# Optimization experiments

Measured on AMD Instinct MI355X. Metric: run time of the kernel, lower is better.

The kernel has to match this reference:

```python
import jax, jax.numpy as jnp
import numpy as np

EPS = 1e-8      # F.normalize eps in _cos_angle
TOPK = 4
DELTA = 1.0     # huber delta
EXTRA_FRAMES = (1, 3, 5, 7)            # teacher-only frames
SHARED = ((2, 1), (4, 2), (6, 3))      # (teacher_idx, student_idx) for shared frames


def _huber(e):
    ae = jnp.abs(e)
    return jnp.where(ae <= DELTA, 0.5 * e * e, DELTA * (ae - 0.5 * DELTA))


def _angles(R, H, Sh):
    # R: [b,r,d] ref, H: [b,r,k,d] sim_high, Sh: [b,s,d] shared.
    # Cosines of the three triplet angles computed via dot-product expansion,
    # avoiding any [b,r,s,k,d] intermediate. cos = (u.v)/(max(|u|,eps)*max(|v|,eps))
    RH  = jnp.einsum('brd,brkd->brk', R, H)
    RSh = jnp.einsum('brd,bsd->brs', R, Sh)
    HSh = jnp.einsum('brkd,bsd->brsk', H, Sh)
    Rn2  = jnp.sum(R * R, -1)        # [b,r]
    Hn2  = jnp.sum(H * H, -1)        # [b,r,k]
    Shn2 = jnp.sum(Sh * Sh, -1)      # [b,s]
    n_RSh = jnp.maximum(jnp.sqrt(jnp.maximum(Rn2[:, :, None] + Shn2[:, None, :] - 2 * RSh, 0.0)), EPS)          # |R-Sh| [b,r,s]
    n_RH  = jnp.maximum(jnp.sqrt(jnp.maximum(Rn2[:, :, None] + Hn2 - 2 * RH, 0.0)), EPS)                        # |R-H|  [b,r,k]
    n_HSh = jnp.maximum(jnp.sqrt(jnp.maximum(Hn2[:, :, None, :] + Shn2[:, None, :, None] - 2 * HSh, 0.0)), EPS) # |H-Sh| [b,r,s,k]
    # angle1: vertex=ref, u=Sh-R, v=H-R
    d1 = HSh - RSh[..., None] - RH[:, :, None, :] + Rn2[:, :, None, None]
    a1 = d1 / (n_RSh[..., None] * n_RH[:, :, None, :])
    # angle2: vertex=H, u=R-H, v=Sh-H
    d2 = RSh[..., None] - RH[:, :, None, :] - HSh + Hn2[:, :, None, :]
    a2 = d2 / (n_RH[:, :, None, :] * n_HSh)
    # angle3: vertex=Sh, u=R-Sh, v=H-Sh
    d3 = RH[:, :, None, :] - RSh[..., None] - HSh + Shn2[:, None, :, None]
    a3 = d3 / (n_RSh[..., None] * n_HSh)
    return a1, a2, a3


def setup_inputs() -> dict:
    key = jax.random.key(0)
    k1, k2, k3, k4 = jax.random.split(key, 4)
    B, S_T, P, D = 2, 8, 2048, 1024
    num_ref, num_shared = 128, 128
    teacher_feats = jax.random.normal(k1, (B, S_T, P, D), jnp.float32)
    student_feats = jax.random.normal(k2, (B, 4, P, D), jnp.float32)
    ref_perm = jax.random.permutation(k3, P)[:num_ref].astype(jnp.int32)
    shared_perm = jax.random.permutation(k4, P)[:num_shared].astype(jnp.int32)
    return {"teacher_feats": teacher_feats, "student_feats": student_feats,
            "ref_perm": ref_perm, "shared_perm": shared_perm}


def reference(teacher_feats, student_feats, ref_perm, shared_perm):
    tf = jax.lax.stop_gradient(teacher_feats)  # teacher is fully detached
    B, _, P, D = tf.shape
    num_ref = ref_perm.shape[0]
    num_shared = shared_perm.shape[0]
    ref_t = tf[:, 0, ref_perm, :]                 # [B,R,D]
    ref_s = student_feats[:, 0, ref_perm, :]
    # teacher-only frames, concatenated along patch dim -> [B, EP, D]
    extra = tf[:, jnp.array(EXTRA_FRAMES), :, :].reshape(B, -1, D)
    # cosine-similarity retrieval (selection_mode='topk')
    rtn = ref_t / jnp.maximum(jnp.linalg.norm(ref_t, axis=-1, keepdims=True), 1e-12)
    etn = extra / jnp.maximum(jnp.linalg.norm(extra, axis=-1, keepdims=True), 1e-12)
    sim = jnp.einsum('brd,bed->bre', rtn, etn)
    _, idx = jax.lax.top_k(sim, TOPK)             # [B,R,K]
    H = jnp.take_along_axis(extra, idx.reshape(B, -1, 1), axis=1).reshape(B, num_ref, TOPK, D)
    s1 = s2 = s3 = jnp.float32(0.0)
    for tidx, sidx in SHARED:
        Sh_t = tf[:, tidx, shared_perm, :]
        Sh_s = student_feats[:, sidx, shared_perm, :]
        a1t, a2t, a3t = _angles(ref_t, H, Sh_t)
        a1s, a2s, a3s = _angles(ref_s, H, Sh_s)
        s1 = s1 + _huber(a1s - a1t).sum()
        s2 = s2 + _huber(a2s - a2t).sum()
        s3 = s3 + _huber(a3s - a3t).sum()
    total = jnp.float32(len(SHARED) * B * num_ref * num_shared * TOPK)
    # angle weights all 1.0
    loss = s1 / total + s2 / total + s3 / total
    return loss
```

## Files before the change

### kernel.cpp

```cpp
#include <hip/hip_runtime.h>
#include <cstdint>
#include <cstddef>
#include <cfloat>
#include <climits>

#define D_DIM   1024
#define P_DIM   2048
#define NB      2
#define NR      128
#define NS      128
#define KTOP    4
#define E_DIM   8192
#define ANG_EPS 1e-8f
#define M_PAIR  768
#define N_PAIR  768

#define SIM_SLICES  4
#define SIM_KSLICE  256
#define PAIR_SLICES 4
#define PAIR_KSLICE 256
#define PAIR_STAGES 16

#define TOPK_DELTA  1.0f
#define MAXCAND     128

typedef short short8 __attribute__((ext_vector_type(8)));
typedef float f32x4 __attribute__((ext_vector_type(4)));

__device__ __forceinline__ float dot4(float4 a, float4 b) {
  return a.x * b.x + a.y * b.y + a.z * b.z + a.w * b.w;
}

__device__ __forceinline__ float huber(float e) {
  float ae = fabsf(e);
  return ae <= 1.0f ? 0.5f * e * e : ae - 0.5f;
}

__device__ __forceinline__ bool better(float va, int ia, float vb, int ib) {
  return (va > vb) || (va == vb && ia < ib);
}

__device__ __forceinline__ unsigned int f2bf(float x) {
  union { float f; unsigned int u; } v; v.f = x;
  unsigned int r = v.u + 0x7fffu + ((v.u >> 16) & 1u);
  return r >> 16;
}
__device__ __forceinline__ unsigned int pk2bf(float x, float y) {
  return f2bf(x) | (f2bf(y) << 16);
}

__device__ __forceinline__ float block_reduce_sum(float v, float* scratch) {
  #pragma unroll
  for (int o = 32; o > 0; o >>= 1) v += __shfl_down(v, o);
  __syncthreads();
  if ((threadIdx.x & 63) == 0) scratch[threadIdx.x >> 6] = v;
  __syncthreads();
  float r = 0.0f;
  int nw = (int)(blockDim.x >> 6);
  if ((int)threadIdx.x < nw) r = scratch[threadIdx.x];
  #pragma unroll
  for (int o = 2; o > 0; o >>= 1) r += __shfl_down(r, o);
  return r;
}

__global__ __launch_bounds__(256) void sim_gemm_kernel(const float* __restrict__ tf,
                                                       const int* __restrict__ ref_perm,
                                                       float* __restrict__ simP,
                                                       float* __restrict__ bn2P) {
  __shared__ unsigned int Ah[128 * 20];
  __shared__ unsigned int Bh[128 * 20];
  __shared__ const float* Arow[128];
  __shared__ const float* Brow[128];
  const int tid = threadIdx.x;
  const int b = blockIdx.z;
  const int slice = blockIdx.y;
  const int nbase = blockIdx.x * 128;
  const int kbase = slice * SIM_KSLICE;
  if (tid < 128) {
    Arow[tid] = tf + ((size_t)(b * 8) * P_DIM + ref_perm[tid]) * D_DIM + kbase;
  } else {
    int n = nbase + (tid - 128);
    Brow[tid - 128] = tf + ((size_t)(b * 8 + 1 + 2 * (n >> 11)) * P_DIM + (n & (P_DIM - 1))) * D_DIM + kbase;
  }
  __syncthreads();

  const int srow = tid >> 1;
  const int shalf = (tid & 1) * 16;
  const float* asrc = Arow[srow] + shalf;
  const float* bsrc = Brow[srow] + shalf;

  float4 av[4], bv[4];
  #pragma unroll
  for (int i = 0; i < 4; ++i) {
    av[i] = *(const float4*)(asrc + 4 * i);
    bv[i] = *(const float4*)(bsrc + 4 * i);
  }

  const int wave = tid >> 6;
  const int lane = tid & 63;
  const int fr = lane & 15;
  const int q16 = (lane >> 4) * 16;
  const char* Ab = (const char*)Ah;
  const char* Bb = (const char*)Bh;

  f32x4 acc[2][8];
  #pragma unroll
  for (int mt = 0; mt < 2; ++mt)
    #pragma unroll
    for (int nt = 0; nt < 8; ++nt)
      #pragma unroll
      for (int r = 0; r < 4; ++r) acc[mt][nt][r] = 0.0f;

  float bn2 = 0.0f;
  unsigned int* adst = Ah + srow * 20 + (tid & 1) * 8;
  unsigned int* bdst = Bh + srow * 20 + (tid & 1) * 8;

  for (int ck = 0; ck < 8; ++ck) {
    bn2 += dot4(bv[0], bv[0]) + dot4(bv[1], bv[1]) + dot4(bv[2], bv[2]) + dot4(bv[3], bv[3]);
    unsigned int ua[8], ub[8];
    #pragma unroll
    for (int i = 0; i < 4; ++i) {
      ua[2 * i]     = pk2bf(av[i].x, av[i].y);
      ua[2 * i + 1] = pk2bf(av[i].z, av[i].w);
      ub[2 * i]     = pk2bf(bv[i].x, bv[i].y);
      ub[2 * i + 1] = pk2bf(bv[i].z, bv[i].w);
    }
    __syncthreads();
    *(uint4*)(adst)     = make_uint4(ua[0], ua[1], ua[2], ua[3]);
    *(uint4*)(adst + 4) = make_uint4(ua[4], ua[5], ua[6], ua[7]);
    *(uint4*)(bdst)     = make_uint4(ub[0], ub[1], ub[2], ub[3]);
    *(uint4*)(bdst + 4) = make_uint4(ub[4], ub[5], ub[6], ub[7]);
    __syncthreads();
    if (ck < 7) {
      const float* an = asrc + (ck + 1) * 32;
      const float* bn = bsrc + (ck + 1) * 32;
      #pragma unroll
      for (int i = 0; i < 4; ++i) {
        av[i] = *(const float4*)(an + 4 * i);
        bv[i] = *(const float4*)(bn + 4 * i);
      }
    }
    short8 afr[2], bfr[8];
    #pragma unroll
    for (int mt = 0; mt < 2; ++mt)
      afr[mt] = *(const short8*)(Ab + (wave * 32 + mt * 16 + fr) * 80 + q16);
    #pragma unroll
    for (int nt = 0; nt < 8; ++nt)
      bfr[nt] = *(const short8*)(Bb + (nt * 16 + fr) * 80 + q16);
    #pragma unroll
    for (int mt = 0; mt < 2; ++mt)
      #pragma unroll
      for (int nt = 0; nt < 8; ++nt)
        acc[mt][nt] = __builtin_amdgcn_mfma_f32_16x16x32_bf16(afr[mt], bfr[nt], acc[mt][nt], 0, 0, 0);
  }

  bn2 += __shfl_xor(bn2, 1);
  if ((tid & 1) == 0)
    bn2P[((size_t)slice * NB + b) * E_DIM + nbase + srow] = bn2;

  float* base = simP + (((size_t)slice * NB + b) * NR) * E_DIM + nbase;
  const int crow = (lane >> 4) * 4;
  #pragma unroll
  for (int mt = 0; mt < 2; ++mt) {
    #pragma unroll
    for (int nt = 0; nt < 8; ++nt) {
      int col = nt * 16 + fr;
      #pragma unroll
      for (int r = 0; r < 4; ++r) {
        int m = wave * 32 + mt * 16 + crow + r;
        base[(size_t)m * E_DIM + col] = acc[mt][nt][r];
      }
    }
  }
}

__global__ __launch_bounds__(256) void topk_kernel(const float* __restrict__ simP,
                                                   const float* __restrict__ bn2P,
                                                   const float* __restrict__ tf,
                                                   const int* __restrict__ ref_perm,
                                                   int* __restrict__ tki) {
  __shared__ float scores[E_DIM];
  __shared__ float sv[1024];
  __shared__ int si[1024];
  __shared__ float candVal[MAXCAND];
  __shared__ int candIdx[MAXCAND];
  __shared__ int cnt;
  const int tid = threadIdx.x;
  const int br = blockIdx.x;
  const int b = br >> 7;
  const int r = br & 127;
  const size_t ST = (size_t)NB * NR * E_DIM;
  const size_t SN = (size_t)NB * E_DIM;
  const float* p = simP + (size_t)br * E_DIM;
  const float* q = bn2P + (size_t)b * E_DIM;
  if (tid == 0) cnt = 0;

  float tv[4] = {-FLT_MAX, -FLT_MAX, -FLT_MAX, -FLT_MAX};
  int ti[4] = {INT_MAX, INT_MAX, INT_MAX, INT_MAX};
  for (int e4 = tid * 4; e4 < E_DIM; e4 += 1024) {
    float4 s = *(const float4*)(p + e4);
    float4 s1 = *(const float4*)(p + ST + e4);
    float4 s2 = *(const float4*)(p + 2 * ST + e4);
    float4 s3 = *(const float4*)(p + 3 * ST + e4);
    float4 n0 = *(const float4*)(q + e4);
    float4 n1 = *(const float4*)(q + SN + e4);
    float4 n2 = *(const float4*)(q + 2 * SN + e4);
    float4 n3 = *(const float4*)(q + 3 * SN + e4);
    float sj[4] = {s.x + s1.x + s2.x + s3.x, s.y + s1.y + s2.y + s3.y,
                   s.z + s1.z + s2.z + s3.z, s.w + s1.w + s2.w + s3.w};
    float nj[4] = {n0.x + n1.x + n2.x + n3.x, n0.y + n1.y + n2.y + n3.y,
                   n0.z + n1.z + n2.z + n3.z, n0.w + n1.w + n2.w + n3.w};
    #pragma unroll
    for (int j = 0; j < 4; ++j) {
      int e = e4 + j;
      float x = sj[j] * rsqrtf(fmaxf(nj[j], 1e-24f));
      scores[e] = x;
      if (better(x, e, tv[3], ti[3])) {
        tv[3] = x; ti[3] = e;
        #pragma unroll
        for (int k = 3; k > 0; --k) {
          if (better(tv[k], ti[k], tv[k - 1], ti[k - 1])) {
            float fv = tv[k]; tv[k] = tv[k - 1]; tv[k - 1] = fv;
            int fi2 = ti[k]; ti[k] = ti[k - 1]; ti[k - 1] = fi2;
          }
        }
      }
    }
  }
  #pragma unroll
  for (int k = 0; k < 4; ++k) { sv[tid * 4 + k] = tv[k]; si[tid * 4 + k] = ti[k]; }
  for (int stride = 128; stride > 0; stride >>= 1) {
    __syncthreads();
    if (tid < stride) {
      float av[4], bv2[4]; int ai[4], bi2[4];
      #pragma unroll
      for (int k = 0; k < 4; ++k) {
        av[k] = sv[tid * 4 + k];               ai[k] = si[tid * 4 + k];
        bv2[k] = sv[(tid + stride) * 4 + k];   bi2[k] = si[(tid + stride) * 4 + k];
      }
      float ov[4]; int oi[4]; int pa = 0, pb = 0;
      #pragma unroll
      for (int k = 0; k < 4; ++k) {
        bool takeA = (pa < 4) && (pb >= 4 || better(av[pa], ai[pa], bv2[pb], bi2[pb]));
        if (takeA) { ov[k] = av[pa]; oi[k] = ai[pa]; ++pa; }
        else       { ov[k] = bv2[pb]; oi[k] = bi2[pb]; ++pb; }
      }
      #pragma unroll
      for (int k = 0; k < 4; ++k) { sv[tid * 4 + k] = ov[k]; si[tid * 4 + k] = oi[k]; }
    }
  }
  __syncthreads();
  const float tau = sv[3] - TOPK_DELTA;

  for (int e4 = tid * 4; e4 < E_DIM; e4 += 1024) {
    #pragma unroll
    for (int j = 0; j < 4; ++j) {
      int e = e4 + j;
      if (scores[e] >= tau) {
        int pos = atomicAdd(&cnt, 1);
        if (pos < MAXCAND) candIdx[pos] = e;
      }
    }
  }
  __syncthreads();
  int cntc = min(cnt, MAXCAND);

  const float* R = tf + ((size_t)(b * 8) * P_DIM + ref_perm[r]) * D_DIM;
  const int wave = tid >> 6;
  const int lane = tid & 63;
  for (int c = wave; c < cntc; c += 4) {
    int e = candIdx[c];
    const float* E = tf + ((size_t)(b * 8 + 1 + 2 * (e >> 11)) * P_DIM + (e & (P_DIM - 1))) * D_DIM;
    float d = 0.0f, n2 = 0.0f;
    #pragma unroll
    for (int i = 0; i < 4; ++i) {
      float4 rv = *(const float4*)(R + lane * 16 + i * 4);
      float4 ev = *(const float4*)(E + lane * 16 + i * 4);
      d += dot4(rv, ev);
      n2 += dot4(ev, ev);
    }
    #pragma unroll
    for (int o = 32; o > 0; o >>= 1) { d += __shfl_xor(d, o); n2 += __shfl_xor(n2, o); }
    if (lane == 0) candVal[c] = d / fmaxf(sqrtf(n2), 1e-12f);
  }
  __syncthreads();
  if (tid == 0) {
    float bv[4] = {-FLT_MAX, -FLT_MAX, -FLT_MAX, -FLT_MAX};
    int bi[4] = {INT_MAX, INT_MAX, INT_MAX, INT_MAX};
    for (int c = 0; c < cntc; ++c) {
      float x = candVal[c]; int e = candIdx[c];
      if (better(x, e, bv[3], bi[3])) {
        bv[3] = x; bi[3] = e;
        #pragma unroll
        for (int k = 3; k > 0; --k) {
          if (better(bv[k], bi[k], bv[k - 1], bi[k - 1])) {
            float fv = bv[k]; bv[k] = bv[k - 1]; bv[k - 1] = fv;
            int fi2 = bi[k]; bi[k] = bi[k - 1]; bi[k - 1] = fi2;
          }
        }
      }
    }
    #pragma unroll
    for (int k = 0; k < 4; ++k) tki[br * 4 + k] = bi[k];
  }
}

__global__ __launch_bounds__(256) void tables_kernel(const float* __restrict__ tf,
                                                     const float* __restrict__ sf,
                                                     const int* __restrict__ ref_perm,
                                                     const int* __restrict__ tki,
                                                     float* __restrict__ rt_n2, float* __restrict__ rs_n2,
                                                     float* __restrict__ hn2,
                                                     float* __restrict__ rh_t, float* __restrict__ rh_s) {
  __shared__ float scr[4];
  int br = blockIdx.x;
  int b = br >> 7, r = br & 127;
  const float* rt = tf + ((size_t)(b * 8) * P_DIM + ref_perm[r]) * D_DIM;
  const float* rs = sf + ((size_t)(b * 4) * P_DIM + ref_perm[r]) * D_DIM;
  int j = threadIdx.x * 4;
  float4 vt = *(const float4*)(rt + j);
  float4 vs = *(const float4*)(rs + j);
  float red;
  red = block_reduce_sum(dot4(vt, vt), scr); if (threadIdx.x == 0) rt_n2[br] = red;
  red = block_reduce_sum(dot4(vs, vs), scr); if (threadIdx.x == 0) rs_n2[br] = red;
  for (int k = 0; k < KTOP; ++k) {
    int e = tki[br * KTOP + k];
    const float* hp = tf + ((size_t)(b * 8 + 1 + 2 * (e >> 11)) * P_DIM + (e & (P_DIM - 1))) * D_DIM;
    float4 vh = *(const float4*)(hp + j);
    red = block_reduce_sum(dot4(vh, vh), scr); if (threadIdx.x == 0) hn2[br * KTOP + k] = red;
    red = block_reduce_sum(dot4(vt, vh), scr); if (threadIdx.x == 0) rh_t[br * KTOP + k] = red;
    red = block_reduce_sum(dot4(vs, vh), scr); if (threadIdx.x == 0) rh_s[br * KTOP + k] = red;
  }
}

__global__ __launch_bounds__(256) void sh_norms_kernel(const float* __restrict__ tf,
                                                       const float* __restrict__ sf,
                                                       const int* __restrict__ shared_perm,
                                                       float* __restrict__ shn2_t,
                                                       float* __restrict__ shn2_s) {
  __shared__ float scr[4];
  int row = blockIdx.x;
  int s = row & 127;
  int side = (row >> 7) & 1;
  int b = (row >> 8) & 1;
  int p = row >> 9;
  const float* ptr = (side == 0)
      ? tf + ((size_t)(b * 8 + 2 * p + 2) * P_DIM + shared_perm[s]) * D_DIM
      : sf + ((size_t)(b * 4 + p + 1) * P_DIM + shared_perm[s]) * D_DIM;
  float4 v = *(const float4*)(ptr + threadIdx.x * 4);
  float red = block_reduce_sum(dot4(v, v), scr);
  if (threadIdx.x == 0) {
    float* dst = (side == 0) ? shn2_t : shn2_s;
    dst[(p * 2 + b) * NS + s] = red;
  }
}

__global__ __launch_bounds__(256) void pair_gemm_kernel(const float* __restrict__ tf,
                                                        const float* __restrict__ sf,
                                                        const int* __restrict__ ref_perm,
                                                        const int* __restrict__ shared_perm,
                                                        const int* __restrict__ tki,
                                                        float* __restrict__ CpP) {
  __shared__ float As[2][16][128];
  __shared__ float Bs[2][16][68];
  __shared__ const float* Arow[128];
  __shared__ const float* Brow[64];
  const int tid = threadIdx.x;
  const int b = blockIdx.z & 1;
  const int slice = blockIdx.z >> 1;
  const int mbase = blockIdx.y * 128;
  const int nbase = blockIdx.x * 64;
  const int kbase = slice * PAIR_KSLICE;
  if (tid < 128) {
    int m = mbase + tid;
    const float* p;
    if (m < 128) {
      p = tf + ((size_t)(b * 8) * P_DIM + ref_perm[m]) * D_DIM;
    } else if (m < 256) {
      p = sf + ((size_t)(b * 4) * P_DIM + ref_perm[m - 128]) * D_DIM;
    } else {
      int h = m - 256, r = h >> 2, k = h & 3;
      int e = tki[(b * NR + r) * KTOP + k];
      p = tf + ((size_t)(b * 8 + 1 + 2 * (e >> 11)) * P_DIM + (e & (P_DIM - 1))) * D_DIM;
    }
    Arow[tid] = p + kbase;
  } else if (tid < 192) {
    int n = nbase + (tid - 128);
    int pr = n >> 8, rem = n & 255, side = rem >> 7, s = rem & 127;
    const float* p;
    if (side == 0) p = tf + ((size_t)(b * 8 + 2 * pr + 2) * P_DIM + shared_perm[s]) * D_DIM;
    else           p = sf + ((size_t)(b * 4 + pr + 1) * P_DIM + shared_perm[s]) * D_DIM;
    Brow[tid - 128] = p + kbase;
  }
  __syncthreads();
  const int rowA = tid & 127;
  const int h8   = (tid >> 7) * 8;
  const int rowB = tid >> 2;
  const int lfB  = (tid & 3) * 4;
  const float* ap = Arow[rowA] + h8;
  const float* bp = Brow[rowB] + lfB;
  float4 a0 = *(const float4*)(ap);
  float4 a1 = *(const float4*)(ap + 4);
  float4 b0 = *(const float4*)(bp);

#define STASH(BUF) do { \
    As[BUF][h8 + 0][rowA] = a0.x; As[BUF][h8 + 1][rowA] = a0.y; \
    As[BUF][h8 + 2][rowA] = a0.z; As[BUF][h8 + 3][rowA] = a0.w; \
    As[BUF][h8 + 4][rowA] = a1.x; As[BUF][h8 + 5][rowA] = a1.y; \
    As[BUF][h8 + 6][rowA] = a1.z; As[BUF][h8 + 7][rowA] = a1.w; \
    Bs[BUF][lfB + 0][rowB] = b0.x; Bs[BUF][lfB + 1][rowB] = b0.y; \
    Bs[BUF][lfB + 2][rowB] = b0.z; Bs[BUF][lfB + 3][rowB] = b0.w; \
  } while (0)

  STASH(0);
  __syncthreads();

  const int tm8 = (tid >> 4) * 8;
  const int tn4 = (tid & 15) * 4;
  float acc[8][4] = {};
  for (int s = 0; s < PAIR_STAGES; ++s) {
    const int cur = s & 1;
    const bool more = (s + 1 < PAIR_STAGES);
    if (more) {
      ap += 16; bp += 16;
      a0 = *(const float4*)(ap);
      a1 = *(const float4*)(ap + 4);
      b0 = *(const float4*)(bp);
    }
    #pragma unroll
    for (int kk = 0; kk < 16; ++kk) {
      float4 x0 = *(const float4*)&As[cur][kk][tm8];
      float4 x1 = *(const float4*)&As[cur][kk][tm8 + 4];
      float4 y0 = *(const float4*)&Bs[cur][kk][tn4];
      float av[8] = {x0.x, x0.y, x0.z, x0.w, x1.x, x1.y, x1.z, x1.w};
      float bv[4] = {y0.x, y0.y, y0.z, y0.w};
      #pragma unroll
      for (int i = 0; i < 8; ++i)
        #pragma unroll
        for (int j = 0; j < 4; ++j)
          acc[i][j] = fmaf(av[i], bv[j], acc[i][j]);
    }
    if (more) STASH(cur ^ 1);
    __syncthreads();
  }

  float* base = CpP + (((size_t)slice * NB + b) * M_PAIR + mbase) * N_PAIR + nbase;
  #pragma unroll
  for (int i = 0; i < 8; ++i) {
    float4 o = make_float4(acc[i][0], acc[i][1], acc[i][2], acc[i][3]);
    *(float4*)(base + (size_t)(tm8 + i) * N_PAIR + tn4) = o;
  }
#undef STASH
}

__global__ __launch_bounds__(128) void loss_kernel(const float* __restrict__ CpP,
                                                   const float* __restrict__ rt_n2,
                                                   const float* __restrict__ rs_n2,
                                                   const float* __restrict__ hn2,
                                                   const float* __restrict__ rh_t,
                                                   const float* __restrict__ rh_s,
                                                   const float* __restrict__ shn2_t,
                                                   const float* __restrict__ shn2_s,
                                                   float* __restrict__ acc) {
  __shared__ float scr[2];
  int r = blockIdx.x, b = blockIdx.y, p = blockIdx.z;
  int s = threadIdx.x;
  int br = b * NR + r;
  const size_t SLC = (size_t)NB * M_PAIR * N_PAIR;
  const float* Cb = CpP + (size_t)b * M_PAIR * N_PAIR;
  auto sumC = [&](int m, int n) -> float {
    const float* q = Cb + (size_t)m * N_PAIR + n;
    float v = 0.0f;
    #pragma unroll
    for (int sl = 0; sl < PAIR_SLICES; ++sl) v += q[sl * SLC];
    return v;
  };
  float Rt2 = rt_n2[br], Rs2 = rs_n2[br];
  float St2 = shn2_t[(p * 2 + b) * NS + s];
  float Ss2 = shn2_s[(p * 2 + b) * NS + s];
  float RSt = sumC(r, p * 256 + s);
  float RSs = sumC(128 + r, p * 256 + 128 + s);
  float sum = 0.0f;
  #pragma unroll
  for (int k = 0; k < KTOP; ++k) {
    float H2 = hn2[br * KTOP + k];
    float RHt = rh_t[br * KTOP + k];
    float RHs = rh_s[br * KTOP + k];
    float HSt = sumC(256 + r * 4 + k, p * 256 + s);
    float HSs = sumC(256 + r * 4 + k, p * 256 + 128 + s);
    float nRSt = fmaxf(sqrtf(fmaxf(Rt2 + St2 - 2.0f * RSt, 0.0f)), ANG_EPS);
    float nRHt = fmaxf(sqrtf(fmaxf(Rt2 + H2 - 2.0f * RHt, 0.0f)), ANG_EPS);
    float nHSt = fmaxf(sqrtf(fmaxf(H2 + St2 - 2.0f * HSt, 0.0f)), ANG_EPS);
    float a1t = (HSt - RSt - RHt + Rt2) / (nRSt * nRHt);
    float a2t = (RSt - RHt - HSt + H2) / (nRHt * nHSt);
    float a3t = (RHt - RSt - HSt + St2) / (nRSt * nHSt);
    float nRSs = fmaxf(sqrtf(fmaxf(Rs2 + Ss2 - 2.0f * RSs, 0.0f)), ANG_EPS);
    float nRHs = fmaxf(sqrtf(fmaxf(Rs2 + H2 - 2.0f * RHs, 0.0f)), ANG_EPS);
    float nHSs = fmaxf(sqrtf(fmaxf(H2 + Ss2 - 2.0f * HSs, 0.0f)), ANG_EPS);
    float a1s = (HSs - RSs - RHs + Rs2) / (nRSs * nRHs);
    float a2s = (RSs - RHs - HSs + H2) / (nRHs * nHSs);
    float a3s = (RHs - RSs - HSs + Ss2) / (nRSs * nHSs);
    sum += huber(a1s - a1t) + huber(a2s - a2t) + huber(a3s - a3t);
  }
  float tot = block_reduce_sum(sum, scr);
  if (threadIdx.x == 0) atomicAdd(acc, tot);
}

__global__ void finalize_kernel(const float* __restrict__ acc, float* __restrict__ out) {
  if (threadIdx.x == 0 && blockIdx.x == 0)
    out[0] = acc[0] * (1.0f / 393216.0f);
}

extern "C" void kernel_launch(void* const* d_in, const int* in_sizes, int n_in,
                              void* d_out, int out_size, void* d_ws, size_t ws_size,
                              hipStream_t stream) {
  const float* tf = (const float*)d_in[0];
  const float* sf = (const float*)d_in[1];
  const int* ref_perm = (const int*)d_in[2];
  const int* shared_perm = (const int*)d_in[3];
  float* ws = (float*)d_ws;

  float* simP   = ws;
  float* bn2P   = simP + (size_t)SIM_SLICES * NB * NR * E_DIM;
  float* CpP    = bn2P + (size_t)SIM_SLICES * NB * E_DIM;
  float* rt_n2  = CpP  + (size_t)PAIR_SLICES * NB * M_PAIR * N_PAIR;
  float* rs_n2  = rt_n2  + NB * NR;
  float* hn2    = rs_n2  + NB * NR;
  float* rh_t   = hn2    + NB * NR * KTOP;
  float* rh_s   = rh_t   + NB * NR * KTOP;
  float* shn2_t = rh_s   + NB * NR * KTOP;
  float* shn2_s = shn2_t + 3 * NB * NS;
  float* acc    = shn2_s + 3 * NB * NS;
  int*   tki    = (int*)(acc + 4);
  float* out = (float*)d_out;

  hipMemsetAsync(acc, 0, sizeof(float), stream);
  sim_gemm_kernel<<<dim3(E_DIM / 128, SIM_SLICES, NB), 256, 0, stream>>>(tf, ref_perm, simP, bn2P);
  topk_kernel<<<NB * NR, 256, 0, stream>>>(simP, bn2P, tf, ref_perm, tki);
  tables_kernel<<<NB * NR, 256, 0, stream>>>(tf, sf, ref_perm, tki, rt_n2, rs_n2, hn2, rh_t, rh_s);
  sh_norms_kernel<<<3 * NB * 2 * NS, 256, 0, stream>>>(tf, sf, shared_perm, shn2_t, shn2_s);
  pair_gemm_kernel<<<dim3(N_PAIR / 64, M_PAIR / 128, NB * PAIR_SLICES), 256, 0, stream>>>(tf, sf, ref_perm, shared_perm, tki, CpP);
  loss_kernel<<<dim3(NR, NB, 3), 128, 0, stream>>>(CpP, rt_n2, rs_n2, hn2, rh_t, rh_s, shn2_t, shn2_s, acc);
  finalize_kernel<<<1, 64, 0, stream>>>(acc, out);
}
```

Before: 343.5 us.

## Move pair GEMM to bf16 MFMA, fuse tables into topk, narrow topk margin

Rewrites the pair GEMM from an fp32 FMA register-tiled loop to bf16 MFMA 16x16x32 with 128x128 tiles, and doubles the K-split to 8 slices of 128. The separate tables kernel is folded into topk_kernel, with each wave computing the norms and dot products for one top-k candidate through shuffle reductions, which saves a launch and re-reading the rows. TOPK_DELTA is reduced from 1.0 to 0.25, shrinking the candidate margin used in refinement. The bf16 pair products lose precision, which the cosine differences may amplify, and the smaller delta risks missing true top-k candidates.

```diff
diff --git a/kernel.cpp b/kernel.cpp
--- a/kernel.cpp
+++ b/kernel.cpp
@@ -17,11 +17,10 @@
 
 #define SIM_SLICES  4
 #define SIM_KSLICE  256
-#define PAIR_SLICES 4
-#define PAIR_KSLICE 256
-#define PAIR_STAGES 16
-
-#define TOPK_DELTA  1.0f
+#define PAIR_SLICES 8
+#define PAIR_KSLICE 128
+
+#define TOPK_DELTA  0.25f
 #define MAXCAND     128
 
 typedef short short8 __attribute__((ext_vector_type(8)));
@@ -177,14 +176,21 @@
 __global__ __launch_bounds__(256) void topk_kernel(const float* __restrict__ simP,
                                                    const float* __restrict__ bn2P,
                                                    const float* __restrict__ tf,
+                                                   const float* __restrict__ sf,
                                                    const int* __restrict__ ref_perm,
-                                                   int* __restrict__ tki) {
+                                                   int* __restrict__ tki,
+                                                   float* __restrict__ rt_n2,
+                                                   float* __restrict__ rs_n2,
+                                                   float* __restrict__ hn2,
+                                                   float* __restrict__ rh_t,
+                                                   float* __restrict__ rh_s) {
   __shared__ float scores[E_DIM];
   __shared__ float sv[1024];
   __shared__ int si[1024];
   __shared__ float candVal[MAXCAND];
   __shared__ int candIdx[MAXCAND];
   __shared__ int cnt;
+  __shared__ int fin4[4];
   const int tid = threadIdx.x;
   const int br = blockIdx.x;
   const int b = br >> 7;
@@ -301,35 +307,41 @@
       }
     }
     #pragma unroll
-    for (int k = 0; k < 4; ++k) tki[br * 4 + k] = bi[k];
-  }
-}
-
-__global__ __launch_bounds__(256) void tables_kernel(const float* __restrict__ tf,
-                                                     const float* __restrict__ sf,
-                                                     const int* __restrict__ ref_perm,
-                                                     const int* __restrict__ tki,
-                                                     float* __restrict__ rt_n2, float* __restrict__ rs_n2,
-                                                     float* __restrict__ hn2,
-                                                     float* __restrict__ rh_t, float* __restrict__ rh_s) {
-  __shared__ float scr[4];
-  int br = blockIdx.x;
-  int b = br >> 7, r = br & 127;
-  const float* rt = tf + ((size_t)(b * 8) * P_DIM + ref_perm[r]) * D_DIM;
-  const float* rs = sf + ((size_t)(b * 4) * P_DIM + ref_perm[r]) * D_DIM;
-  int j = threadIdx.x * 4;
-  float4 vt = *(const float4*)(rt + j);
-  float4 vs = *(const float4*)(rs + j);
-  float red;
-  red = block_reduce_sum(dot4(vt, vt), scr); if (threadIdx.x == 0) rt_n2[br] = red;
-  red = block_reduce_sum(dot4(vs, vs), scr); if (threadIdx.x == 0) rs_n2[br] = red;
-  for (int k = 0; k < KTOP; ++k) {
-    int e = tki[br * KTOP + k];
-    const float* hp = tf + ((size_t)(b * 8 + 1 + 2 * (e >> 11)) * P_DIM + (e & (P_DIM - 1))) * D_DIM;
-    float4 vh = *(const float4*)(hp + j);
-    red = block_reduce_sum(dot4(vh, vh), scr); if (threadIdx.x == 0) hn2[br * KTOP + k] = red;
-    red = block_reduce_sum(dot4(vt, vh), scr); if (threadIdx.x == 0) rh_t[br * KTOP + k] = red;
-    red = block_reduce_sum(dot4(vs, vh), scr); if (threadIdx.x == 0) rh_s[br * KTOP + k] = red;
+    for (int k = 0; k < 4; ++k) { tki[br * 4 + k] = bi[k]; fin4[k] = bi[k]; }
+  }
+  __syncthreads();
+
+  {
+    const float* RS = sf + ((size_t)(b * 4) * P_DIM + ref_perm[r]) * D_DIM;
+    int e = fin4[wave];
+    const float* H = tf + ((size_t)(b * 8 + 1 + 2 * (e >> 11)) * P_DIM + (e & (P_DIM - 1))) * D_DIM;
+    float h2 = 0.0f, rht = 0.0f, rhs = 0.0f, rtn = 0.0f, rsn = 0.0f;
+    #pragma unroll
+    for (int i = 0; i < 4; ++i) {
+      float4 rv = *(const float4*)(R + lane * 16 + i * 4);
+      float4 sv2 = *(const float4*)(RS + lane * 16 + i * 4);
+      float4 hv = *(const float4*)(H + lane * 16 + i * 4);
+      h2 += dot4(hv, hv);
+      rht += dot4(rv, hv);
+      rhs += dot4(sv2, hv);
+      rtn += dot4(rv, rv);
+      rsn += dot4(sv2, sv2);
+    }
+    #pragma unroll
+    for (int o = 32; o > 0; o >>= 1) {
+      h2 += __shfl_xor(h2, o);
+      rht += __shfl_xor(rht, o);
+      rhs += __shfl_xor(rhs, o);
+      rtn += __shfl_xor(rtn, o);
+      rsn += __shfl_xor(rsn, o);
+    }
+    if (lane == 0) {
+      hn2[br * KTOP + wave] = h2;
+      rh_t[br * KTOP + wave] = rht;
+      rh_s[br * KTOP + wave] = rhs;
+      if (wave == 0) rt_n2[br] = rtn;
+      if (wave == 1) rs_n2[br] = rsn;
+    }
   }
 }
 
@@ -361,15 +373,15 @@
                                                         const int* __restrict__ shared_perm,
                                                         const int* __restrict__ tki,
                                                         float* __restrict__ CpP) {
-  __shared__ float As[2][16][128];
-  __shared__ float Bs[2][16][68];
+  __shared__ unsigned int Ah[128 * 20];
+  __shared__ unsigned int Bh[128 * 20];
   __shared__ const float* Arow[128];
-  __shared__ const float* Brow[64];
+  __shared__ const float* Brow[128];
   const int tid = threadIdx.x;
   const int b = blockIdx.z & 1;
   const int slice = blockIdx.z >> 1;
   const int mbase = blockIdx.y * 128;
-  const int nbase = blockIdx.x * 64;
+  const int nbase = blockIdx.x * 128;
   const int kbase = slice * PAIR_KSLICE;
   if (tid < 128) {
     int m = mbase + tid;
@@ -384,7 +396,7 @@
       p = tf + ((size_t)(b * 8 + 1 + 2 * (e >> 11)) * P_DIM + (e & (P_DIM - 1))) * D_DIM;
     }
     Arow[tid] = p + kbase;
-  } else if (tid < 192) {
+  } else {
     int n = nbase + (tid - 128);
     int pr = n >> 8, rem = n & 255, side = rem >> 7, s = rem & 127;
     const float* p;
@@ -393,64 +405,89 @@
     Brow[tid - 128] = p + kbase;
   }
   __syncthreads();
-  const int rowA = tid & 127;
-  const int h8   = (tid >> 7) * 8;
-  const int rowB = tid >> 2;
-  const int lfB  = (tid & 3) * 4;
-  const float* ap = Arow[rowA] + h8;
-  const float* bp = Brow[rowB] + lfB;
-  float4 a0 = *(const float4*)(ap);
-  float4 a1 = *(const float4*)(ap + 4);
-  float4 b0 = *(const float4*)(bp);
-
-#define STASH(BUF) do { \
-    As[BUF][h8 + 0][rowA] = a0.x; As[BUF][h8 + 1][rowA] = a0.y; \
-    As[BUF][h8 + 2][rowA] = a0.z; As[BUF][h8 + 3][rowA] = a0.w; \
-    As[BUF][h8 + 4][rowA] = a1.x; As[BUF][h8 + 5][rowA] = a1.y; \
-    As[BUF][h8 + 6][rowA] = a1.z; As[BUF][h8 + 7][rowA] = a1.w; \
-    Bs[BUF][lfB + 0][rowB] = b0.x; Bs[BUF][lfB + 1][rowB] = b0.y; \
-    Bs[BUF][lfB + 2][rowB] = b0.z; Bs[BUF][lfB + 3][rowB] = b0.w; \
-  } while (0)
-
-  STASH(0);
-  __syncthreads();
-
-  const int tm8 = (tid >> 4) * 8;
-  const int tn4 = (tid & 15) * 4;
-  float acc[8][4] = {};
-  for (int s = 0; s < PAIR_STAGES; ++s) {
-    const int cur = s & 1;
-    const bool more = (s + 1 < PAIR_STAGES);
-    if (more) {
-      ap += 16; bp += 16;
-      a0 = *(const float4*)(ap);
-      a1 = *(const float4*)(ap + 4);
-      b0 = *(const float4*)(bp);
-    }
-    #pragma unroll
-    for (int kk = 0; kk < 16; ++kk) {
-      float4 x0 = *(const float4*)&As[cur][kk][tm8];
-      float4 x1 = *(const float4*)&As[cur][kk][tm8 + 4];
-      float4 y0 = *(const float4*)&Bs[cur][kk][tn4];
-      float av[8] = {x0.x, x0.y, x0.z, x0.w, x1.x, x1.y, x1.z, x1.w};
-      float bv[4] = {y0.x, y0.y, y0.z, y0.w};
-      #pragma unroll
-      for (int i = 0; i < 8; ++i)
-        #pragma unroll
-        for (int j = 0; j < 4; ++j)
-          acc[i][j] = fmaf(av[i], bv[j], acc[i][j]);
-    }
-    if (more) STASH(cur ^ 1);
+
+  const int srow = tid >> 1;
+  const int shalf = (tid & 1) * 16;
+  const float* asrc = Arow[srow] + shalf;
+  const float* bsrc = Brow[srow] + shalf;
+
+  float4 av[4], bv[4];
+  #pragma unroll
+  for (int i = 0; i < 4; ++i) {
+    av[i] = *(const float4*)(asrc + 4 * i);
+    bv[i] = *(const float4*)(bsrc + 4 * i);
+  }
+
+  const int wave = tid >> 6;
+  const int lane = tid & 63;
+  const int fr = lane & 15;
+  const int q16 = (lane >> 4) * 16;
+  const char* Ab = (const char*)Ah;
+  const char* Bb = (const char*)Bh;
+
+  f32x4 acc[2][8];
+  #pragma unroll
+  for (int mt = 0; mt < 2; ++mt)
+    #pragma unroll
+    for (int nt = 0; nt < 8; ++nt)
+      #pragma unroll
+      for (int r = 0; r < 4; ++r) acc[mt][nt][r] = 0.0f;
+
+  unsigned int* adst = Ah + srow * 20 + (tid & 1) * 8;
+  unsigned int* bdst = Bh + srow * 20 + (tid & 1) * 8;
+
+  for (int ck = 0; ck < 4; ++ck) {
+    unsigned int ua[8], ub[8];
+    #pragma unroll
+    for (int i = 0; i < 4; ++i) {
+      ua[2 * i]     = pk2bf(av[i].x, av[i].y);
+      ua[2 * i + 1] = pk2bf(av[i].z, av[i].w);
+      ub[2 * i]     = pk2bf(bv[i].x, bv[i].y);
+      ub[2 * i + 1] = pk2bf(bv[i].z, bv[i].w);
+    }
     __syncthreads();
+    *(uint4*)(adst)     = make_uint4(ua[0], ua[1], ua[2], ua[3]);
+    *(uint4*)(adst + 4) = make_uint4(ua[4], ua[5], ua[6], ua[7]);
+    *(uint4*)(bdst)     = make_uint4(ub[0], ub[1], ub[2], ub[3]);
+    *(uint4*)(bdst + 4) = make_uint4(ub[4], ub[5], ub[6], ub[7]);
+    __syncthreads();
+    if (ck < 3) {
+      const float* an = asrc + (ck + 1) * 32;
+      const float* bn = bsrc + (ck + 1) * 32;
+      #pragma unroll
+      for (int i = 0; i < 4; ++i) {
+        av[i] = *(const float4*)(an + 4 * i);
+        bv[i] = *(const float4*)(bn + 4 * i);
+      }
+    }
+    short8 afr[2], bfr[8];
+    #pragma unroll
+    for (int mt = 0; mt < 2; ++mt)
+      afr[mt] = *(const short8*)(Ab + (wave * 32 + mt * 16 + fr) * 80 + q16);
+    #pragma unroll
+    for (int nt = 0; nt < 8; ++nt)
+      bfr[nt] = *(const short8*)(Bb + (nt * 16 + fr) * 80 + q16);
+    #pragma unroll
+    for (int mt = 0; mt < 2; ++mt)
+      #pragma unroll
+      for (int nt = 0; nt < 8; ++nt)
+        acc[mt][nt] = __builtin_amdgcn_mfma_f32_16x16x32_bf16(afr[mt], bfr[nt], acc[mt][nt], 0, 0, 0);
   }
 
   float* base = CpP + (((size_t)slice * NB + b) * M_PAIR + mbase) * N_PAIR + nbase;
-  #pragma unroll
-  for (int i = 0; i < 8; ++i) {
-    float4 o = make_float4(acc[i][0], acc[i][1], acc[i][2], acc[i][3]);
-    *(float4*)(base + (size_t)(tm8 + i) * N_PAIR + tn4) = o;
-  }
-#undef STASH
+  const int crow = (lane >> 4) * 4;
+  #pragma unroll
+  for (int mt = 0; mt < 2; ++mt) {
+    #pragma unroll
+    for (int nt = 0; nt < 8; ++nt) {
+      int col = nt * 16 + fr;
+      #pragma unroll
+      for (int r = 0; r < 4; ++r) {
+        int m = wave * 32 + mt * 16 + crow + r;
+        base[(size_t)m * N_PAIR + col] = acc[mt][nt][r];
+      }
+    }
+  }
 }
 
 __global__ __launch_bounds__(128) void loss_kernel(const float* __restrict__ CpP,
@@ -536,10 +573,10 @@
 
   hipMemsetAsync(acc, 0, sizeof(float), stream);
   sim_gemm_kernel<<<dim3(E_DIM / 128, SIM_SLICES, NB), 256, 0, stream>>>(tf, ref_perm, simP, bn2P);
-  topk_kernel<<<NB * NR, 256, 0, stream>>>(simP, bn2P, tf, ref_perm, tki);
-  tables_kernel<<<NB * NR, 256, 0, stream>>>(tf, sf, ref_perm, tki, rt_n2, rs_n2, hn2, rh_t, rh_s);
+  topk_kernel<<<NB * NR, 256, 0, stream>>>(simP, bn2P, tf, sf, ref_perm, tki,
+                                           rt_n2, rs_n2, hn2, rh_t, rh_s);
   sh_norms_kernel<<<3 * NB * 2 * NS, 256, 0, stream>>>(tf, sf, shared_perm, shn2_t, shn2_s);
-  pair_gemm_kernel<<<dim3(N_PAIR / 64, M_PAIR / 128, NB * PAIR_SLICES), 256, 0, stream>>>(tf, sf, ref_perm, shared_perm, tki, CpP);
+  pair_gemm_kernel<<<dim3(N_PAIR / 128, M_PAIR / 128, NB * PAIR_SLICES), 256, 0, stream>>>(tf, sf, ref_perm, shared_perm, tki, CpP);
   loss_kernel<<<dim3(NR, NB, 3), 128, 0, stream>>>(CpP, rt_n2, rs_n2, hn2, rh_t, rh_s, shn2_t, shn2_s, acc);
   finalize_kernel<<<1, 64, 0, stream>>>(acc, out);
 }
```

Measured after the change: 281.4 us. -18.1%, faster.
